# Kernel tuning notes

Measured on AMD Instinct MI355X. Metric: run time of the kernel, lower is better.

## Reference

```python
import jax, jax.numpy as jnp
import numpy as np

GAMMA = 10.0   # RBF width of the stand-in radial kernel
EPS = 1e-12    # safe-norm epsilon (avoids NaN grad at zero difference)

N_POINTS = 16384
N_NBR = 32
C_IN = 16
C_OUT = 16
N_BASIS = 16


def setup_inputs() -> dict:
    key = jax.random.key(0)
    k1, k2, k3, k4, k5, k6 = jax.random.split(key, 6)
    inp = jax.random.normal(k1, (C_IN, N_POINTS), dtype=jnp.float32)
    coords = jax.random.normal(k2, (N_POINTS, 3), dtype=jnp.float32)
    W = jax.random.normal(k3, (C_OUT, C_IN, N_BASIS), dtype=jnp.float32)
    centers = jax.random.uniform(k4, (N_BASIS,), dtype=jnp.float32)
    relative_mask = jax.random.uniform(k5, (N_POINTS, N_NBR), dtype=jnp.float32)
    neighbors = jax.random.randint(k6, (N_POINTS, N_NBR), 0, N_POINTS)
    return {"input": inp, "coords": coords, "W": W, "centers": centers,
            "relative_mask": relative_mask, "neighbors": neighbors}


def reference(input, coords, W, centers, relative_mask, neighbors):
    # difference_matrix: [N, K, 3]
    diff = coords[neighbors] - coords[:, None, :]
    # edge length with safe sqrt: [N, K]
    r = jnp.sqrt(jnp.sum(diff * diff, axis=-1) + EPS)
    # Gaussian radial basis: [N, K, B]
    rbf = jnp.exp(-GAMMA * (r[..., None] - centers) ** 2)
    # per-edge kernel: [C_out, C_in, N, K]
    kernel = jnp.einsum('oib,nkb->oink', W, rbf)
    # relative_mask applied as einsum 'ba,dcba->dcba'
    kernel = relative_mask * kernel
    # neighbor feature gather: [C_in, N, K]
    neighbors_input = input[:, neighbors]
    # contraction 'cba,dcba->db': [C_out, N]
    output = jnp.einsum('ink,oink->on', neighbors_input, kernel)
    return output
```

## Files before the change

### kernel.cpp

```cpp
#include <hip/hip_runtime.h>
#include <hip/hip_bf16.h>

#define NPTS 16384
#define NNBR 32
#define CIN 16
#define COUT 16
#define NBASIS 16

#define WF_OS 264
#define ML_PS 264

typedef _Float16 half8 __attribute__((ext_vector_type(8)));
typedef unsigned short ushort8 __attribute__((ext_vector_type(8)));
typedef float floatx4 __attribute__((ext_vector_type(4)));

__global__ __launch_bounds__(256) void transpose_kernel(
        const float* __restrict__ input, float* __restrict__ xT) {
    const int n = blockIdx.x * 256 + threadIdx.x;
    float v[CIN];
    #pragma unroll
    for (int i = 0; i < CIN; ++i) v[i] = input[i * NPTS + n];
    float4* dst = (float4*)&xT[n * CIN];
    #pragma unroll
    for (int j = 0; j < 4; ++j)
        dst[j] = make_float4(v[4 * j], v[4 * j + 1], v[4 * j + 2], v[4 * j + 3]);
}

__global__ __launch_bounds__(256) void se3_conv_kernel(
        const float* __restrict__ xT,
        const float* __restrict__ coords,
        const float* __restrict__ W,
        const float* __restrict__ centers,
        const float* __restrict__ mask,
        const int* __restrict__ neighbors,
        float* __restrict__ out) {
    __shared__ _Float16 Wf[COUT * WF_OS];
    __shared__ _Float16 Mld[16 * ML_PS];
    __shared__ float    rs[16 * NNBR];
    __shared__ unsigned short nb16[16 * NNBR];
    __shared__ _Float16 mv16[16 * NNBR];

    const int tid = threadIdx.x;
    const int t = tid & 15;
    const int quad = (tid >> 4) & 3;
    const int wv = tid >> 6;
    const int nbase = blockIdx.x * 16;

    {
        const int o = tid >> 4, b = tid & 15;
        _Float16 wrow[16];
        #pragma unroll
        for (int i = 0; i < CIN; ++i)
            wrow[i] = (_Float16)W[o * 256 + i * 16 + b];
        *(half8*)&Wf[o * WF_OS + b * 16]     = *(half8*)&wrow[0];
        *(half8*)&Wf[o * WF_OS + b * 16 + 8] = *(half8*)&wrow[8];
    }

    #pragma unroll
    for (int s = 0; s < 2; ++s) {
        const int f = tid + s * 256;
        const int pt = f >> 5;
        const int n = nbase + pt;
        const int nbr = neighbors[nbase * NNBR + f] & (NPTS - 1);
        const float m = mask[nbase * NNBR + f];
        const float dx = coords[nbr * 3 + 0] - coords[n * 3 + 0];
        const float dy = coords[nbr * 3 + 1] - coords[n * 3 + 1];
        const float dz = coords[nbr * 3 + 2] - coords[n * 3 + 2];
        rs[f] = sqrtf(dx * dx + dy * dy + dz * dz + 1e-12f);
        nb16[f] = (unsigned short)nbr;
        mv16[f] = (_Float16)m;
    }
    __syncthreads();

    const float cb = centers[t];
    const int pbase = wv * 4;
    #pragma unroll
    for (int q = 0; q < 4; ++q) {
        const int pq = pbase + q;
        const int kb = pq * NNBR + 8 * quad;
        const float4 r0 = *(const float4*)&rs[kb];
        const float4 r1 = *(const float4*)&rs[kb + 4];
        const ushort8 nbv = *(const ushort8*)&nb16[kb];
        const half8 mvv = *(const half8*)&mv16[kb];
        const float rj[8] = {r0.x, r0.y, r0.z, r0.w, r1.x, r1.y, r1.z, r1.w};
        half8 af, bf;
        #pragma unroll
        for (int j = 0; j < 8; ++j) {
            const float d = rj[j] - cb;
            bf[j] = (_Float16)__expf(-10.0f * d * d);
            const float x = xT[(int)nbv[j] * CIN + t];
            af[j] = (_Float16)(x * (float)mvv[j]);
        }
        floatx4 c = {0.0f, 0.0f, 0.0f, 0.0f};
        c = __builtin_amdgcn_mfma_f32_16x16x32_f16(af, bf, c, 0, 0, 0);
        _Float16 h[4];
        #pragma unroll
        for (int v = 0; v < 4; ++v) h[v] = (_Float16)c[v];
        *(uint2*)&Mld[pq * ML_PS + t * 16 + 4 * quad] = *(uint2*)h;
    }
    __syncthreads();

    floatx4 acc = {0.0f, 0.0f, 0.0f, 0.0f};
    #pragma unroll
    for (int cch = 0; cch < 8; ++cch) {
        const int bi = cch * 32 + 8 * quad;
        const half8 a = *(const half8*)&Wf[t * WF_OS + bi];
        const half8 b = *(const half8*)&Mld[t * ML_PS + bi];
        acc = __builtin_amdgcn_mfma_f32_16x16x32_f16(a, b, acc, 0, 0, 0);
    }
    if (wv == (t >> 2)) {
        #pragma unroll
        for (int v = 0; v < 4; ++v)
            out[(4 * quad + v) * NPTS + nbase + t] = acc[v];
    }
}

extern "C" void kernel_launch(void* const* d_in, const int* in_sizes, int n_in,
                              void* d_out, int out_size, void* d_ws, size_t ws_size,
                              hipStream_t stream) {
    const float* input   = (const float*)d_in[0];
    const float* coords  = (const float*)d_in[1];
    const float* W       = (const float*)d_in[2];
    const float* centers = (const float*)d_in[3];
    const float* mask    = (const float*)d_in[4];
    const int*   nbr     = (const int*)d_in[5];
    float* out = (float*)d_out;

    float* xT = (float*)d_ws;
    transpose_kernel<<<NPTS / 256, 256, 0, stream>>>(input, xT);
    se3_conv_kernel<<<NPTS / 16, 256, 0, stream>>>(xT, coords, W, centers,
                                                   mask, nbr, out);
}
```

Baseline: 75.77 us.

## Precompute fp16 features, padded coords and fp16 weights; compute edges inline per lane

The prep kernel now stores the transposed input as fp16, writes the coordinates padded to float4, and converts W to fp16 once. The conv kernel drops the shared-memory staging of distances, neighbor indices and mask, along with its first barrier. Each lane now loads neighbors and mask as vectors and computes edge lengths inline from float4 coordinate gathers. This halves the gather bytes for features and removes a sync, at the cost of redundant distance computation across the 16 channel lanes and more scattered global loads per lane.

```diff
diff --git a/kernel.cpp b/kernel.cpp
--- a/kernel.cpp
+++ b/kernel.cpp
@@ -11,34 +11,41 @@
 #define ML_PS 264
 
 typedef _Float16 half8 __attribute__((ext_vector_type(8)));
-typedef unsigned short ushort8 __attribute__((ext_vector_type(8)));
 typedef float floatx4 __attribute__((ext_vector_type(4)));
 
-__global__ __launch_bounds__(256) void transpose_kernel(
-        const float* __restrict__ input, float* __restrict__ xT) {
+#define WS_XT 0
+#define WS_C4 (NPTS * CIN)
+#define WS_WF (WS_C4 + NPTS * 4 * 2)
+
+__global__ __launch_bounds__(256) void prep_kernel(
+        const float* __restrict__ input, const float* __restrict__ coords,
+        const float* __restrict__ W, _Float16* __restrict__ ws) {
     const int n = blockIdx.x * 256 + threadIdx.x;
-    float v[CIN];
+    _Float16 v[CIN];
     #pragma unroll
-    for (int i = 0; i < CIN; ++i) v[i] = input[i * NPTS + n];
-    float4* dst = (float4*)&xT[n * CIN];
-    #pragma unroll
-    for (int j = 0; j < 4; ++j)
-        dst[j] = make_float4(v[4 * j], v[4 * j + 1], v[4 * j + 2], v[4 * j + 3]);
+    for (int i = 0; i < CIN; ++i) v[i] = (_Float16)input[i * NPTS + n];
+    *(half8*)&ws[WS_XT + n * CIN]     = *(half8*)&v[0];
+    *(half8*)&ws[WS_XT + n * CIN + 8] = *(half8*)&v[8];
+    float4* c4 = (float4*)&ws[WS_C4];
+    c4[n] = make_float4(coords[n * 3 + 0], coords[n * 3 + 1], coords[n * 3 + 2], 0.0f);
+    if (blockIdx.x == 0) {
+        const int o = threadIdx.x >> 4, b = threadIdx.x & 15;
+        _Float16 w[16];
+        #pragma unroll
+        for (int i = 0; i < CIN; ++i) w[i] = (_Float16)W[o * 256 + i * 16 + b];
+        *(half8*)&ws[WS_WF + o * 256 + b * 16]     = *(half8*)&w[0];
+        *(half8*)&ws[WS_WF + o * 256 + b * 16 + 8] = *(half8*)&w[8];
+    }
 }
 
 __global__ __launch_bounds__(256) void se3_conv_kernel(
-        const float* __restrict__ xT,
-        const float* __restrict__ coords,
-        const float* __restrict__ W,
+        const _Float16* __restrict__ ws,
         const float* __restrict__ centers,
         const float* __restrict__ mask,
         const int* __restrict__ neighbors,
         float* __restrict__ out) {
     __shared__ _Float16 Wf[COUT * WF_OS];
     __shared__ _Float16 Mld[16 * ML_PS];
-    __shared__ float    rs[16 * NNBR];
-    __shared__ unsigned short nb16[16 * NNBR];
-    __shared__ _Float16 mv16[16 * NNBR];
 
     const int tid = threadIdx.x;
     const int t = tid & 15;
@@ -46,50 +53,43 @@
     const int wv = tid >> 6;
     const int nbase = blockIdx.x * 16;
 
+    const _Float16* xT16 = &ws[WS_XT];
+    const float4* coords4 = (const float4*)&ws[WS_C4];
+
     {
-        const int o = tid >> 4, b = tid & 15;
-        _Float16 wrow[16];
-        #pragma unroll
-        for (int i = 0; i < CIN; ++i)
-            wrow[i] = (_Float16)W[o * 256 + i * 16 + b];
-        *(half8*)&Wf[o * WF_OS + b * 16]     = *(half8*)&wrow[0];
-        *(half8*)&Wf[o * WF_OS + b * 16 + 8] = *(half8*)&wrow[8];
+        const int o = tid >> 4, ch = tid & 15;
+        const half8 w0 = *(const half8*)&ws[WS_WF + o * 256 + ch * 16];
+        const half8 w1 = *(const half8*)&ws[WS_WF + o * 256 + ch * 16 + 8];
+        *(half8*)&Wf[o * WF_OS + ch * 16]     = w0;
+        *(half8*)&Wf[o * WF_OS + ch * 16 + 8] = w1;
     }
 
-    #pragma unroll
-    for (int s = 0; s < 2; ++s) {
-        const int f = tid + s * 256;
-        const int pt = f >> 5;
-        const int n = nbase + pt;
-        const int nbr = neighbors[nbase * NNBR + f] & (NPTS - 1);
-        const float m = mask[nbase * NNBR + f];
-        const float dx = coords[nbr * 3 + 0] - coords[n * 3 + 0];
-        const float dy = coords[nbr * 3 + 1] - coords[n * 3 + 1];
-        const float dz = coords[nbr * 3 + 2] - coords[n * 3 + 2];
-        rs[f] = sqrtf(dx * dx + dy * dy + dz * dz + 1e-12f);
-        nb16[f] = (unsigned short)nbr;
-        mv16[f] = (_Float16)m;
-    }
-    __syncthreads();
-
     const float cb = centers[t];
-    const int pbase = wv * 4;
     #pragma unroll
     for (int q = 0; q < 4; ++q) {
-        const int pq = pbase + q;
-        const int kb = pq * NNBR + 8 * quad;
-        const float4 r0 = *(const float4*)&rs[kb];
-        const float4 r1 = *(const float4*)&rs[kb + 4];
-        const ushort8 nbv = *(const ushort8*)&nb16[kb];
-        const half8 mvv = *(const half8*)&mv16[kb];
-        const float rj[8] = {r0.x, r0.y, r0.z, r0.w, r1.x, r1.y, r1.z, r1.w};
+        const int pq = wv * 4 + q;
+        const int n = nbase + pq;
+        const int kb = n * NNBR + 8 * quad;
+        const int4 n0 = *(const int4*)&neighbors[kb];
+        const int4 n1 = *(const int4*)&neighbors[kb + 4];
+        const float4 m0 = *(const float4*)&mask[kb];
+        const float4 m1 = *(const float4*)&mask[kb + 4];
+        const float4 cc = coords4[n];
+        const int nb[8] = {n0.x & (NPTS - 1), n0.y & (NPTS - 1),
+                           n0.z & (NPTS - 1), n0.w & (NPTS - 1),
+                           n1.x & (NPTS - 1), n1.y & (NPTS - 1),
+                           n1.z & (NPTS - 1), n1.w & (NPTS - 1)};
+        const float mj[8] = {m0.x, m0.y, m0.z, m0.w, m1.x, m1.y, m1.z, m1.w};
         half8 af, bf;
         #pragma unroll
         for (int j = 0; j < 8; ++j) {
-            const float d = rj[j] - cb;
+            const float4 cj = coords4[nb[j]];
+            const float dx = cj.x - cc.x, dy = cj.y - cc.y, dz = cj.z - cc.z;
+            const float r = sqrtf(dx * dx + dy * dy + dz * dz + 1e-12f);
+            const float d = r - cb;
             bf[j] = (_Float16)__expf(-10.0f * d * d);
-            const float x = xT[(int)nbv[j] * CIN + t];
-            af[j] = (_Float16)(x * (float)mvv[j]);
+            const float x = (float)xT16[nb[j] * CIN + t];
+            af[j] = (_Float16)(x * mj[j]);
         }
         floatx4 c = {0.0f, 0.0f, 0.0f, 0.0f};
         c = __builtin_amdgcn_mfma_f32_16x16x32_f16(af, bf, c, 0, 0, 0);
@@ -125,9 +125,8 @@
     const float* mask    = (const float*)d_in[4];
     const int*   nbr     = (const int*)d_in[5];
     float* out = (float*)d_out;
+    _Float16* ws = (_Float16*)d_ws;
 
-    float* xT = (float*)d_ws;
-    transpose_kernel<<<NPTS / 256, 256, 0, stream>>>(input, xT);
-    se3_conv_kernel<<<NPTS / 16, 256, 0, stream>>>(xT, coords, W, centers,
-                                                   mask, nbr, out);
+    prep_kernel<<<NPTS / 256, 256, 0, stream>>>(input, coords, W, ws);
+    se3_conv_kernel<<<NPTS / 16, 256, 0, stream>>>(ws, centers, mask, nbr, out);
 }
```

Result: no change. 76.89 us (+1.5%).
